# Kernel tuning notes

Hardware: AMD Instinct MI355X
Metric: run time of the kernel (lower is better)

The kernel has to match this reference:

```python
import jax, jax.numpy as jnp
import numpy as np
from jax import lax

B, T, D = 32, 512, 1024
H = 1024
R = 64


def setup_inputs() -> dict:
    key = jax.random.key(0)
    ks = jax.random.split(key, 14)
    s = lambda *sh: 1.0 / np.sqrt(sh[-1])
    inp = {
        "x": jax.random.normal(ks[0], (B, T, D), jnp.float32),
        # sLSTM block params (input_dim=D -> hidden H)
        "Ws": jax.random.normal(ks[1], (4 * H, D), jnp.float32) * s(4 * H, D),
        "bWs": jax.random.normal(ks[2], (4 * H,), jnp.float32) * 0.01,
        "Us": jax.random.normal(ks[3], (4 * H, H), jnp.float32) * s(4 * H, H),
        "bUs": jax.random.normal(ks[4], (4 * H,), jnp.float32) * 0.01,
        "alpha": jnp.ones((H,), jnp.float32),
        # mLSTM block params (input dim = H after first block)
        "Wm": jax.random.normal(ks[5], (4 * H, H), jnp.float32) * s(4 * H, H),
        "bWm": jax.random.normal(ks[6], (4 * H,), jnp.float32) * 0.01,
        "Um": jax.random.normal(ks[7], (4 * H, H), jnp.float32) * s(4 * H, H),
        "bUm": jax.random.normal(ks[8], (4 * H,), jnp.float32) * 0.01,
        "A": jax.random.normal(ks[9], (R, H), jnp.float32) * s(R, H),
        "Bm": jax.random.normal(ks[10], (R, H), jnp.float32) * s(R, H),
        "P": jax.random.normal(ks[11], (H, R), jnp.float32) * s(H, R),
    }
    return inp


def _gates(z):
    i, f, o, g = jnp.split(z, 4, axis=-1)
    return jax.nn.sigmoid(i), jax.nn.sigmoid(f), jax.nn.sigmoid(o), jnp.tanh(g)


def _slstm(x, W, bW, U, bU, alpha):
    b = x.shape[0]
    h0 = jnp.zeros((b, H), x.dtype)
    c0 = jnp.zeros((b, H), x.dtype)
    # precompute the input projection for all timesteps: [T, B, 4H]
    xw = jnp.einsum('btd,kd->tbk', x, W) + bW

    def step(carry, xw_t):
        h, c = carry
        i, f, o, g = _gates(xw_t + h @ U.T + bU)
        c = alpha * (f * c + i * g)
        h = o * jnp.tanh(c)
        return (h, c), h

    _, hs = lax.scan(step, (h0, c0), xw)
    return jnp.swapaxes(hs, 0, 1)  # [B, T, H]


def _mlstm(x, W, bW, U, bU, A, Bm, P):
    b = x.shape[0]
    h0 = jnp.zeros((b, H), x.dtype)
    c0 = jnp.zeros((b, H), x.dtype)
    xw = jnp.einsum('btd,kd->tbk', x, W) + bW     # [T, B, 4H]
    xa = jnp.einsum('btd,rd->tbr', x, A)          # [T, B, R]

    def step(carry, inputs):
        h, c = carry
        xw_t, xa_t = inputs
        i, f, o, g = _gates(xw_t + h @ U.T + bU)
        mix = (xa_t * (h @ Bm.T)) @ P.T           # low-rank mixing -> [B, H]
        c = f * c + i * g + 0.1 * mix
        h = o * jnp.tanh(c)
        return (h, c), h

    _, hs = lax.scan(step, (h0, c0), (xw, xa))
    return jnp.swapaxes(hs, 0, 1)  # [B, T, H]


def reference(x, Ws, bWs, Us, bUs, alpha, Wm, bWm, Um, bUm, A, Bm, P):
    out = _slstm(x, Ws, bWs, Us, bUs, alpha)
    out = _mlstm(out, Wm, bWm, Um, bUm, A, Bm, P)
    return out
```

## Files before the change

### kernel.cpp

```cpp
#include <hip/hip_runtime.h>

#define BB   32
#define TT_  512
#define DD   1024
#define HH   1024
#define RR_  64
#define FH   4096
#define TC   32

typedef __attribute__((ext_vector_type(8))) short          bf16x8;
typedef __attribute__((ext_vector_type(4))) float          f32x4;
typedef __attribute__((ext_vector_type(4))) unsigned short us4;

__device__ __forceinline__ unsigned short f2bf(float x) {
    union { float f; unsigned u; } v; v.f = x;
    return (unsigned short)((v.u + 0x7FFFu + ((v.u >> 16) & 1u)) >> 16);
}

__global__ void init_zero(float4* p, int n4) {
    int i = blockIdx.x * blockDim.x + threadIdx.x;
    if (i < n4) p[i] = make_float4(0.f, 0.f, 0.f, 0.f);
}

__global__ void cvt_bf16(const float* __restrict__ src,
                         unsigned short* __restrict__ dst, int n4) {
    int i = blockIdx.x * blockDim.x + threadIdx.x;
    int stride = gridDim.x * blockDim.x;
    for (; i < n4; i += stride) {
        float4 v = ((const float4*)src)[i];
        us4 t; t.x = f2bf(v.x); t.y = f2bf(v.y); t.z = f2bf(v.z); t.w = f2bf(v.w);
        ((us4*)dst)[i] = t;
    }
}

template<int BM, int BN>
__global__ __launch_bounds__(256) void gemm_mfma(
    const float* __restrict__ Abase, long strideT, long strideB,
    const float* __restrict__ W, const float* __restrict__ bias,
    float* __restrict__ C, int M, int N, int K)
{
    constexpr int BK  = 32;
    constexpr int WTM = BM / 2, WTN = BN / 2;
    constexpr int MI  = WTM / 16, NI = WTN / 16;
    constexpr int AU  = BM * (BK / 4) / 256;
    constexpr int BU  = BN * (BK / 4) / 256;

    __shared__ __align__(16) unsigned short As[BM * BK];
    __shared__ __align__(16) unsigned short Bs[BN * BK];

    const int tid  = threadIdx.x;
    const int lane = tid & 63, wave = tid >> 6;
    const int wm   = wave >> 1, wn = wave & 1;
    const int kg   = lane >> 4;
    const int lr   = lane & 15;
    const long bm  = (long)blockIdx.y * BM;
    const long bn  = (long)blockIdx.x * BN;

    const float* ag[AU]; int alds[AU];
    const float* bg[BU]; int blds[BU];
#pragma unroll
    for (int i = 0; i < AU; ++i) {
        int u = i * 256 + tid, row = u >> 3, uc = u & 7;
        long m = bm + row;
        ag[i]   = Abase + (m >> 5) * strideT + (m & 31) * strideB + uc * 4;
        alds[i] = row * BK + uc * 4;
    }
#pragma unroll
    for (int i = 0; i < BU; ++i) {
        int u = i * 256 + tid, row = u >> 3, uc = u & 7;
        bg[i]   = W + (long)(bn + row) * K + uc * 4;
        blds[i] = row * BK + uc * 4;
    }

    f32x4 acc[MI][NI] = {};

    float4 av[AU], bv[BU];
#pragma unroll
    for (int i = 0; i < AU; ++i) av[i] = *(const float4*)(ag[i]);
#pragma unroll
    for (int i = 0; i < BU; ++i) bv[i] = *(const float4*)(bg[i]);

    for (int k0 = 0; k0 < K; k0 += BK) {
        __syncthreads();
#pragma unroll
        for (int i = 0; i < AU; ++i) {
            us4 t; t.x = f2bf(av[i].x); t.y = f2bf(av[i].y);
                   t.z = f2bf(av[i].z); t.w = f2bf(av[i].w);
            *(us4*)&As[alds[i]] = t;
        }
#pragma unroll
        for (int i = 0; i < BU; ++i) {
            us4 t; t.x = f2bf(bv[i].x); t.y = f2bf(bv[i].y);
                   t.z = f2bf(bv[i].z); t.w = f2bf(bv[i].w);
            *(us4*)&Bs[blds[i]] = t;
        }
        __syncthreads();

        if (k0 + BK < K) {
#pragma unroll
            for (int i = 0; i < AU; ++i) av[i] = *(const float4*)(ag[i] + k0 + BK);
#pragma unroll
            for (int i = 0; i < BU; ++i) bv[i] = *(const float4*)(bg[i] + k0 + BK);
        }

        bf16x8 af[MI], bfr[NI];
#pragma unroll
        for (int mi = 0; mi < MI; ++mi)
            af[mi] = *(const bf16x8*)&As[(wm * WTM + mi * 16 + lr) * BK + kg * 8];
#pragma unroll
        for (int ni = 0; ni < NI; ++ni)
            bfr[ni] = *(const bf16x8*)&Bs[(wn * WTN + ni * 16 + lr) * BK + kg * 8];
#pragma unroll
        for (int mi = 0; mi < MI; ++mi)
#pragma unroll
            for (int ni = 0; ni < NI; ++ni)
                acc[mi][ni] = __builtin_amdgcn_mfma_f32_16x16x32_bf16(
                    af[mi], bfr[ni], acc[mi][ni], 0, 0, 0);
    }

    const int rbase = (lane >> 4) * 4;
#pragma unroll
    for (int mi = 0; mi < MI; ++mi) {
        long m0 = bm + wm * WTM + mi * 16 + rbase;
        long tt = m0 >> 5; int bq = (int)(m0 & 31);
#pragma unroll
        for (int ni = 0; ni < NI; ++ni) {
            long n = bn + wn * WTN + ni * 16 + lr;
            float bia = bias ? bias[n] : 0.f;
            float4 v = make_float4(acc[mi][ni][0] + bia, acc[mi][ni][1] + bia,
                                   acc[mi][ni][2] + bia, acc[mi][ni][3] + bia);
            *(float4*)&C[(tt * N + n) * 32 + bq] = v;
        }
    }
}

__device__ __forceinline__ void slstm_body(
    int bx, const float* __restrict__ xwT,
    const unsigned short* __restrict__ Ubf, const float* __restrict__ bU,
    const float* __restrict__ alpha, const unsigned short* __restrict__ hin,
    unsigned short* __restrict__ hout, float* __restrict__ cst,
    float* __restrict__ out1t, char* smem)
{
    unsigned short* hs = (unsigned short*)smem;
    float* zsl = (float*)(smem + 65536);
    const int tid  = threadIdx.x;
    const int lane = tid & 63, wv = tid >> 6;
    const int j0   = bx * 16;
    const int lr   = lane & 15;
    const int koff = (lane >> 4) << 3;

    const uint4* hg = (const uint4*)hin;
#pragma unroll
    for (int i = 0; i < 16; ++i) {
        int u = tid + (i << 8);
        int o = u << 4;
        int sw = o ^ (((o >> 11) & 7) << 4);
        *(uint4*)(smem + sw) = hg[u];
    }
    __syncthreads();

    const unsigned short* Arow = Ubf + (((long)(wv * HH + j0 + lr)) << 10) + koff;
    const int base0 = lr * 2048 + koff * 2;
    const int base1 = (lr + 16) * 2048 + koff * 2;
    const int swz   = (lr & 7) << 4;

    f32x4 accZ0 = {0.f, 0.f, 0.f, 0.f}, accZ1 = {0.f, 0.f, 0.f, 0.f};
#pragma unroll 4
    for (int k0 = 0; k0 < 1024; k0 += 32) {
        bf16x8 a  = *(const bf16x8*)(Arow + k0);
        bf16x8 b0 = *(const bf16x8*)(smem + ((base0 + k0 * 2) ^ swz));
        bf16x8 b1 = *(const bf16x8*)(smem + ((base1 + k0 * 2) ^ swz));
        accZ0 = __builtin_amdgcn_mfma_f32_16x16x32_bf16(a, b0, accZ0, 0, 0, 0);
        accZ1 = __builtin_amdgcn_mfma_f32_16x16x32_bf16(a, b1, accZ1, 0, 0, 0);
    }
#pragma unroll
    for (int r = 0; r < 4; ++r) {
        int jj = ((lane >> 4) << 2) + r;
        zsl[wv * 512 + jj * 32 + lr]      = accZ0[r];
        zsl[wv * 512 + jj * 32 + lr + 16] = accZ1[r];
    }
    __syncthreads();

#pragma unroll
    for (int rep = 0; rep < 2; ++rep) {
        int p = (rep << 8) + tid;
        int j = p >> 5, b = p & 31;
        int n0 = j0 + j;
        float zi = xwT[(long)n0 * 32 + b]            + zsl[j * 32 + b]        + bU[n0];
        float zf = xwT[(long)(HH + n0) * 32 + b]     + zsl[512 + j * 32 + b]  + bU[HH + n0];
        float zo = xwT[(long)(2 * HH + n0) * 32 + b] + zsl[1024 + j * 32 + b] + bU[2 * HH + n0];
        float zg = xwT[(long)(3 * HH + n0) * 32 + b] + zsl[1536 + j * 32 + b] + bU[3 * HH + n0];
        float ig = 1.f / (1.f + expf(-zi));
        float fg = 1.f / (1.f + expf(-zf));
        float og = 1.f / (1.f + expf(-zo));
        float g  = tanhf(zg);
        float cold = cst[(long)b * HH + n0];
        float cn = alpha[n0] * (fg * cold + ig * g);
        float hn = og * tanhf(cn);
        cst[(long)b * HH + n0]  = cn;
        hout[(long)b * HH + n0] = f2bf(hn);
        out1t[(long)b * HH + n0] = hn;
    }
}

__device__ __forceinline__ void mlstm_body(
    int bx, const float* __restrict__ xwT,
    const unsigned short* __restrict__ Ubf, const float* __restrict__ bU,
    const float* __restrict__ Pmat, const unsigned short* __restrict__ Bmbf,
    const float* __restrict__ xaT, const unsigned short* __restrict__ hin,
    unsigned short* __restrict__ hout, float* __restrict__ cst,
    float* __restrict__ out, int t, char* smem)
{
    unsigned short* hs = (unsigned short*)smem;
    float* zsl = (float*)(smem + 65536);
    float* ssl = (float*)(smem + 65536 + 8192);
    const int tid  = threadIdx.x;
    const int lane = tid & 63, wv = tid >> 6;
    const int j0   = bx * 16;
    const int lr   = lane & 15;
    const int koff = (lane >> 4) << 3;

    const uint4* hg = (const uint4*)hin;
#pragma unroll
    for (int i = 0; i < 16; ++i) {
        int u = tid + (i << 8);
        int o = u << 4;
        int sw = o ^ (((o >> 11) & 7) << 4);
        *(uint4*)(smem + sw) = hg[u];
    }
    __syncthreads();

    const unsigned short* Arow = Ubf + (((long)(wv * HH + j0 + lr)) << 10) + koff;
    const unsigned short* Brow = Bmbf + (((long)(wv * 16 + lr)) << 10) + koff;
    const int base0 = lr * 2048 + koff * 2;
    const int base1 = (lr + 16) * 2048 + koff * 2;
    const int swz   = (lr & 7) << 4;

    f32x4 accZ0 = {0.f, 0.f, 0.f, 0.f}, accZ1 = {0.f, 0.f, 0.f, 0.f};
    f32x4 accS0 = {0.f, 0.f, 0.f, 0.f}, accS1 = {0.f, 0.f, 0.f, 0.f};
#pragma unroll 4
    for (int k0 = 0; k0 < 1024; k0 += 32) {
        bf16x8 a  = *(const bf16x8*)(Arow + k0);
        bf16x8 s  = *(const bf16x8*)(Brow + k0);
        bf16x8 b0 = *(const bf16x8*)(smem + ((base0 + k0 * 2) ^ swz));
        bf16x8 b1 = *(const bf16x8*)(smem + ((base1 + k0 * 2) ^ swz));
        accZ0 = __builtin_amdgcn_mfma_f32_16x16x32_bf16(a, b0, accZ0, 0, 0, 0);
        accZ1 = __builtin_amdgcn_mfma_f32_16x16x32_bf16(a, b1, accZ1, 0, 0, 0);
        accS0 = __builtin_amdgcn_mfma_f32_16x16x32_bf16(s, b0, accS0, 0, 0, 0);
        accS1 = __builtin_amdgcn_mfma_f32_16x16x32_bf16(s, b1, accS1, 0, 0, 0);
    }
#pragma unroll
    for (int r = 0; r < 4; ++r) {
        int jj = ((lane >> 4) << 2) + r;
        zsl[wv * 512 + jj * 32 + lr]      = accZ0[r];
        zsl[wv * 512 + jj * 32 + lr + 16] = accZ1[r];
        ssl[(wv * 16 + jj) * 32 + lr]      = accS0[r];
        ssl[(wv * 16 + jj) * 32 + lr + 16] = accS1[r];
    }
    __syncthreads();

#pragma unroll
    for (int i = 0; i < 8; ++i) {
        int idx = tid + (i << 8);
        ssl[idx] *= xaT[idx];
    }
    __syncthreads();

#pragma unroll
    for (int rep = 0; rep < 2; ++rep) {
        int p = (rep << 8) + tid;
        int j = p >> 5, b = p & 31;
        int n0 = j0 + j;
        float zi = xwT[(long)n0 * 32 + b]            + zsl[j * 32 + b]        + bU[n0];
        float zf = xwT[(long)(HH + n0) * 32 + b]     + zsl[512 + j * 32 + b]  + bU[HH + n0];
        float zo = xwT[(long)(2 * HH + n0) * 32 + b] + zsl[1024 + j * 32 + b] + bU[2 * HH + n0];
        float zg = xwT[(long)(3 * HH + n0) * 32 + b] + zsl[1536 + j * 32 + b] + bU[3 * HH + n0];
        float ig = 1.f / (1.f + expf(-zi));
        float fg = 1.f / (1.f + expf(-zf));
        float og = 1.f / (1.f + expf(-zo));
        float g  = tanhf(zg);
        const float* Pj = Pmat + (long)n0 * 64;
        float mx = 0.f;
#pragma unroll
        for (int r = 0; r < 64; ++r) mx += Pj[r] * ssl[r * 32 + b];
        float cold = cst[(long)b * HH + n0];
        float cn = fg * cold + ig * g + 0.1f * mx;
        float hn = og * tanhf(cn);
        cst[(long)b * HH + n0]  = cn;
        hout[(long)b * HH + n0] = f2bf(hn);
        out[(long)b * (TT_ * HH) + (long)t * HH + n0] = hn;
    }
}

__global__ __launch_bounds__(256) void fused_step(
    const float* __restrict__ xwTs, const unsigned short* __restrict__ UbfS,
    const float* __restrict__ bUs, const float* __restrict__ alpha,
    const unsigned short* __restrict__ hsin, unsigned short* __restrict__ hsout,
    float* __restrict__ cS, float* __restrict__ out1t,
    const float* __restrict__ xwTm, const unsigned short* __restrict__ UbfM,
    const float* __restrict__ bUm, const float* __restrict__ Pmat,
    const unsigned short* __restrict__ Bmbf, const float* __restrict__ xaT,
    const unsigned short* __restrict__ hmin, unsigned short* __restrict__ hmout,
    float* __restrict__ cM, float* __restrict__ out, int t,
    int do_s, int do_m)
{
    __shared__ __align__(16) char smem[81920];
    const int bx = blockIdx.x;
    if (bx < 64) {
        if (do_s)
            slstm_body(bx, xwTs, UbfS, bUs, alpha, hsin, hsout, cS, out1t, smem);
    } else {
        if (do_m)
            mlstm_body(bx - 64, xwTm, UbfM, bUm, Pmat, Bmbf, xaT,
                       hmin, hmout, cM, out, t, smem);
    }
}

extern "C" void kernel_launch(void* const* d_in, const int* in_sizes, int n_in,
                              void* d_out, int out_size, void* d_ws, size_t ws_size,
                              hipStream_t stream) {
    const float* x     = (const float*)d_in[0];
    const float* Ws    = (const float*)d_in[1];
    const float* bWs   = (const float*)d_in[2];
    const float* Us    = (const float*)d_in[3];
    const float* bUs   = (const float*)d_in[4];
    const float* alpha = (const float*)d_in[5];
    const float* Wm    = (const float*)d_in[6];
    const float* bWm   = (const float*)d_in[7];
    const float* Um    = (const float*)d_in[8];
    const float* bUm   = (const float*)d_in[9];
    const float* A     = (const float*)d_in[10];
    const float* Bm    = (const float*)d_in[11];
    const float* P     = (const float*)d_in[12];
    float* out = (float*)d_out;

    float* w      = (float*)d_ws;
    float* xwTs   = w;
    float* xwTm   = xwTs + (long)TC * FH * 32;
    float* out1c  = xwTm + (long)TC * FH * 32;
    float* xaT    = out1c + (long)TC * BB * HH;
    unsigned short* UbfS = (unsigned short*)(xaT + (long)TC * RR_ * 32);
    unsigned short* UbfM = UbfS + (long)FH * HH;
    unsigned short* Bmbf = UbfM + (long)FH * HH;
    unsigned short* hbsA = Bmbf + (long)RR_ * HH;
    unsigned short* hbsB = hbsA + BB * HH;
    unsigned short* hbmA = hbsB + BB * HH;
    unsigned short* hbmB = hbmA + BB * HH;
    float* cS     = (float*)(hbmB + BB * HH);
    float* cM     = cS + BB * HH;

    init_zero<<<128, 256, 0, stream>>>((float4*)hbsA, 32768);

    cvt_bf16<<<2048, 256, 0, stream>>>(Us, UbfS, FH * HH / 4);
    cvt_bf16<<<2048, 256, 0, stream>>>(Um, UbfM, FH * HH / 4);
    cvt_bf16<<<64,   256, 0, stream>>>(Bm, Bmbf, RR_ * HH / 4);

    dim3 gbig(FH / 128, (TC * BB) / 64);
    dim3 gxa(RR_ / 64, (TC * BB) / 64);
    const int NC = TT_ / TC;

    for (int ch = 0; ch <= NC; ++ch) {
        const int do_s = (ch < NC), do_m = (ch > 0);

        if (do_s)
            gemm_mfma<64, 128><<<gbig, 256, 0, stream>>>(
                x + (long)(ch * TC) * DD, (long)DD, (long)TT_ * DD, Ws, bWs,
                xwTs, TC * BB, FH, DD);

        for (int tt = 0; tt < TC; ++tt) {
            const unsigned short* hsin = (tt & 1) ? hbsB : hbsA;
            unsigned short* hsout      = (tt & 1) ? hbsA : hbsB;
            const unsigned short* hmin = (tt & 1) ? hbmB : hbmA;
            unsigned short* hmout      = (tt & 1) ? hbmA : hbmB;
            fused_step<<<128, 256, 0, stream>>>(
                xwTs + (long)tt * FH * 32, UbfS, bUs, alpha,
                hsin, hsout, cS, out1c + (long)tt * BB * HH,
                xwTm + (long)tt * FH * 32, UbfM, bUm, P, Bmbf,
                xaT + (long)tt * RR_ * 32,
                hmin, hmout, cM, out, (ch - 1) * TC + tt,
                do_s, do_m);
        }

        if (do_s) {
            gemm_mfma<64, 128><<<gbig, 256, 0, stream>>>(
                out1c, (long)BB * HH, (long)HH, Wm, bWm,
                xwTm, TC * BB, FH, HH);
            gemm_mfma<64, 64><<<gxa, 256, 0, stream>>>(
                out1c, (long)BB * HH, (long)HH, A, nullptr,
                xaT, TC * BB, RR_, HH);
        }
    }
}
```

Baseline: 8.726 ms.

## Pre-convert GEMM operands to bf16 and fuse Wm and A projections into one GEMM

The input-projection GEMMs now read bf16 operands from pre-converted weights (Ws, Wm, A) and a per-chunk bf16 copy of x. The sLSTM step writes its hidden output directly as bf16. The Wm and A projections are concatenated into one padded weight matrix so a single GEMM produces both xw and xa, with xa read at an offset. The GEMM uses BK=64 with XOR-swizzled shared memory to cut per-iteration fp32-to-bf16 conversion and bank conflicts. This adds extra conversion kernels and workspace but reduces per-chunk launches and memory traffic. The recurrence still dominates runtime.

```diff
diff --git a/kernel.cpp b/kernel.cpp
--- a/kernel.cpp
+++ b/kernel.cpp
@@ -7,6 +7,7 @@
 #define RR_  64
 #define FH   4096
 #define TC   32
+#define NCMB 4224
 
 typedef __attribute__((ext_vector_type(8))) short          bf16x8;
 typedef __attribute__((ext_vector_type(4))) float          f32x4;
@@ -33,17 +34,33 @@
     }
 }
 
+__global__ void fill_bcomb(const float* __restrict__ bWm, float* __restrict__ bcomb) {
+    int i = blockIdx.x * blockDim.x + threadIdx.x;
+    if (i < NCMB) bcomb[i] = (i < FH) ? bWm[i] : 0.f;
+}
+
+__global__ void cvt_x_chunk(const float* __restrict__ x,
+                            unsigned short* __restrict__ xbfc, int t0) {
+    int id = blockIdx.x * blockDim.x + threadIdx.x;
+    for (int u = id; u < 32 * 32 * 256; u += 65536) {
+        int d4 = u & 255, b = (u >> 8) & 31, tt = u >> 13;
+        float4 v = *(const float4*)&x[(((long)b * TT_) + t0 + tt) * DD + (d4 << 2)];
+        us4 o; o.x = f2bf(v.x); o.y = f2bf(v.y); o.z = f2bf(v.z); o.w = f2bf(v.w);
+        *(us4*)&xbfc[(((long)tt * 32 + b) << 10) + (d4 << 2)] = o;
+    }
+}
+
 template<int BM, int BN>
-__global__ __launch_bounds__(256) void gemm_mfma(
-    const float* __restrict__ Abase, long strideT, long strideB,
-    const float* __restrict__ W, const float* __restrict__ bias,
-    float* __restrict__ C, int M, int N, int K)
+__global__ __launch_bounds__(256) void gemm_bf(
+    const unsigned short* __restrict__ Abase, long strideT, long strideB,
+    const unsigned short* __restrict__ W, const float* __restrict__ bias,
+    float* __restrict__ C, int N, int K)
 {
-    constexpr int BK  = 32;
+    constexpr int BK  = 64;
     constexpr int WTM = BM / 2, WTN = BN / 2;
     constexpr int MI  = WTM / 16, NI = WTN / 16;
-    constexpr int AU  = BM * (BK / 4) / 256;
-    constexpr int BU  = BN * (BK / 4) / 256;
+    constexpr int AU  = BM * 8 / 256;
+    constexpr int BU  = BN * 8 / 256;
 
     __shared__ __align__(16) unsigned short As[BM * BK];
     __shared__ __align__(16) unsigned short Bs[BN * BK];
@@ -56,66 +73,72 @@
     const long bm  = (long)blockIdx.y * BM;
     const long bn  = (long)blockIdx.x * BN;
 
-    const float* ag[AU]; int alds[AU];
-    const float* bg[BU]; int blds[BU];
+    const unsigned short* ag[AU]; int ast[AU];
+    const unsigned short* bg[BU]; int bst[BU];
 #pragma unroll
     for (int i = 0; i < AU; ++i) {
         int u = i * 256 + tid, row = u >> 3, uc = u & 7;
         long m = bm + row;
-        ag[i]   = Abase + (m >> 5) * strideT + (m & 31) * strideB + uc * 4;
-        alds[i] = row * BK + uc * 4;
+        ag[i]  = Abase + (m >> 5) * strideT + (m & 31) * strideB + uc * 8;
+        ast[i] = (row * 128 + uc * 16) ^ ((row & 7) << 4);
     }
 #pragma unroll
     for (int i = 0; i < BU; ++i) {
         int u = i * 256 + tid, row = u >> 3, uc = u & 7;
-        bg[i]   = W + (long)(bn + row) * K + uc * 4;
-        blds[i] = row * BK + uc * 4;
+        bg[i]  = W + (long)(bn + row) * K + uc * 8;
+        bst[i] = (row * 128 + uc * 16) ^ ((row & 7) << 4);
     }
 
     f32x4 acc[MI][NI] = {};
 
-    float4 av[AU], bv[BU];
-#pragma unroll
-    for (int i = 0; i < AU; ++i) av[i] = *(const float4*)(ag[i]);
-#pragma unroll
-    for (int i = 0; i < BU; ++i) bv[i] = *(const float4*)(bg[i]);
+    uint4 av[AU], bv[BU];
+#pragma unroll
+    for (int i = 0; i < AU; ++i) av[i] = *(const uint4*)(ag[i]);
+#pragma unroll
+    for (int i = 0; i < BU; ++i) bv[i] = *(const uint4*)(bg[i]);
 
     for (int k0 = 0; k0 < K; k0 += BK) {
         __syncthreads();
 #pragma unroll
-        for (int i = 0; i < AU; ++i) {
-            us4 t; t.x = f2bf(av[i].x); t.y = f2bf(av[i].y);
-                   t.z = f2bf(av[i].z); t.w = f2bf(av[i].w);
-            *(us4*)&As[alds[i]] = t;
-        }
-#pragma unroll
-        for (int i = 0; i < BU; ++i) {
-            us4 t; t.x = f2bf(bv[i].x); t.y = f2bf(bv[i].y);
-                   t.z = f2bf(bv[i].z); t.w = f2bf(bv[i].w);
-            *(us4*)&Bs[blds[i]] = t;
-        }
+        for (int i = 0; i < AU; ++i) *(uint4*)((char*)As + ast[i]) = av[i];
+#pragma unroll
+        for (int i = 0; i < BU; ++i) *(uint4*)((char*)Bs + bst[i]) = bv[i];
         __syncthreads();
 
         if (k0 + BK < K) {
 #pragma unroll
-            for (int i = 0; i < AU; ++i) av[i] = *(const float4*)(ag[i] + k0 + BK);
-#pragma unroll
-            for (int i = 0; i < BU; ++i) bv[i] = *(const float4*)(bg[i] + k0 + BK);
-        }
-
-        bf16x8 af[MI], bfr[NI];
-#pragma unroll
-        for (int mi = 0; mi < MI; ++mi)
-            af[mi] = *(const bf16x8*)&As[(wm * WTM + mi * 16 + lr) * BK + kg * 8];
-#pragma unroll
-        for (int ni = 0; ni < NI; ++ni)
-            bfr[ni] = *(const bf16x8*)&Bs[(wn * WTN + ni * 16 + lr) * BK + kg * 8];
-#pragma unroll
-        for (int mi = 0; mi < MI; ++mi)
-#pragma unroll
-            for (int ni = 0; ni < NI; ++ni)
-                acc[mi][ni] = __builtin_amdgcn_mfma_f32_16x16x32_bf16(
-                    af[mi], bfr[ni], acc[mi][ni], 0, 0, 0);
+            for (int i = 0; i < AU; ++i) av[i] = *(const uint4*)(ag[i] + k0 + BK);
+#pragma unroll
+            for (int i = 0; i < BU; ++i) bv[i] = *(const uint4*)(bg[i] + k0 + BK);
+        }
+
+        bf16x8 af[MI][2], bfr[NI][2];
+#pragma unroll
+        for (int mi = 0; mi < MI; ++mi) {
+            int row = wm * WTM + mi * 16 + lr;
+            int rb = row * 128, sw = (row & 7) << 4;
+#pragma unroll
+            for (int kk = 0; kk < 2; ++kk)
+                af[mi][kk] = *(const bf16x8*)((const char*)As +
+                              (rb + ((kk * 64 + kg * 16) ^ sw)));
+        }
+#pragma unroll
+        for (int ni = 0; ni < NI; ++ni) {
+            int row = wn * WTN + ni * 16 + lr;
+            int rb = row * 128, sw = (row & 7) << 4;
+#pragma unroll
+            for (int kk = 0; kk < 2; ++kk)
+                bfr[ni][kk] = *(const bf16x8*)((const char*)Bs +
+                              (rb + ((kk * 64 + kg * 16) ^ sw)));
+        }
+#pragma unroll
+        for (int kk = 0; kk < 2; ++kk)
+#pragma unroll
+            for (int mi = 0; mi < MI; ++mi)
+#pragma unroll
+                for (int ni = 0; ni < NI; ++ni)
+                    acc[mi][ni] = __builtin_amdgcn_mfma_f32_16x16x32_bf16(
+                        af[mi][kk], bfr[ni][kk], acc[mi][ni], 0, 0, 0);
     }
 
     const int rbase = (lane >> 4) * 4;
@@ -139,9 +162,8 @@
     const unsigned short* __restrict__ Ubf, const float* __restrict__ bU,
     const float* __restrict__ alpha, const unsigned short* __restrict__ hin,
     unsigned short* __restrict__ hout, float* __restrict__ cst,
-    float* __restrict__ out1t, char* smem)
+    unsigned short* __restrict__ out1t, char* smem)
 {
-    unsigned short* hs = (unsigned short*)smem;
     float* zsl = (float*)(smem + 65536);
     const int tid  = threadIdx.x;
     const int lane = tid & 63, wv = tid >> 6;
@@ -197,9 +219,10 @@
         float cold = cst[(long)b * HH + n0];
         float cn = alpha[n0] * (fg * cold + ig * g);
         float hn = og * tanhf(cn);
+        unsigned short hb = f2bf(hn);
         cst[(long)b * HH + n0]  = cn;
-        hout[(long)b * HH + n0] = f2bf(hn);
-        out1t[(long)b * HH + n0] = hn;
+        hout[(long)b * HH + n0] = hb;
+        out1t[(long)b * HH + n0] = hb;
     }
 }
 
@@ -207,13 +230,13 @@
     int bx, const float* __restrict__ xwT,
     const unsigned short* __restrict__ Ubf, const float* __restrict__ bU,
     const float* __restrict__ Pmat, const unsigned short* __restrict__ Bmbf,
-    const float* __restrict__ xaT, const unsigned short* __restrict__ hin,
+    const unsigned short* __restrict__ hin,
     unsigned short* __restrict__ hout, float* __restrict__ cst,
     float* __restrict__ out, int t, char* smem)
 {
-    unsigned short* hs = (unsigned short*)smem;
     float* zsl = (float*)(smem + 65536);
     float* ssl = (float*)(smem + 65536 + 8192);
+    const float* xaT = xwT + (long)FH * 32;
     const int tid  = threadIdx.x;
     const int lane = tid & 63, wv = tid >> 6;
     const int j0   = bx * 16;
@@ -296,10 +319,10 @@
     const float* __restrict__ xwTs, const unsigned short* __restrict__ UbfS,
     const float* __restrict__ bUs, const float* __restrict__ alpha,
     const unsigned short* __restrict__ hsin, unsigned short* __restrict__ hsout,
-    float* __restrict__ cS, float* __restrict__ out1t,
+    float* __restrict__ cS, unsigned short* __restrict__ out1t,
     const float* __restrict__ xwTm, const unsigned short* __restrict__ UbfM,
     const float* __restrict__ bUm, const float* __restrict__ Pmat,
-    const unsigned short* __restrict__ Bmbf, const float* __restrict__ xaT,
+    const unsigned short* __restrict__ Bmbf,
     const unsigned short* __restrict__ hmin, unsigned short* __restrict__ hmout,
     float* __restrict__ cM, float* __restrict__ out, int t,
     int do_s, int do_m)
@@ -311,7 +334,7 @@
             slstm_body(bx, xwTs, UbfS, bUs, alpha, hsin, hsout, cS, out1t, smem);
     } else {
         if (do_m)
-            mlstm_body(bx - 64, xwTm, UbfM, bUm, Pmat, Bmbf, xaT,
+            mlstm_body(bx - 64, xwTm, UbfM, bUm, Pmat, Bmbf,
                        hmin, hmout, cM, out, t, smem);
     }
 }
@@ -334,38 +357,46 @@
     const float* P     = (const float*)d_in[12];
     float* out = (float*)d_out;
 
-    float* w      = (float*)d_ws;
-    float* xwTs   = w;
-    float* xwTm   = xwTs + (long)TC * FH * 32;
-    float* out1c  = xwTm + (long)TC * FH * 32;
-    float* xaT    = out1c + (long)TC * BB * HH;
-    unsigned short* UbfS = (unsigned short*)(xaT + (long)TC * RR_ * 32);
-    unsigned short* UbfM = UbfS + (long)FH * HH;
-    unsigned short* Bmbf = UbfM + (long)FH * HH;
+    float* xwTs  = (float*)d_ws;
+    float* xwTm  = xwTs + (long)TC * FH * 32;
+    float* bcomb = xwTm + (long)TC * NCMB * 32;
+    unsigned short* out1c = (unsigned short*)(bcomb + NCMB);
+    unsigned short* xbfc  = out1c + (long)TC * BB * HH;
+    unsigned short* Wsbf  = xbfc + (long)TC * BB * HH;
+    unsigned short* Wcomb = Wsbf + (long)FH * HH;
+    unsigned short* UbfS  = Wcomb + (long)NCMB * HH;
+    unsigned short* UbfM  = UbfS + (long)FH * HH;
+    unsigned short* Bmbf  = UbfM + (long)FH * HH;
     unsigned short* hbsA = Bmbf + (long)RR_ * HH;
     unsigned short* hbsB = hbsA + BB * HH;
     unsigned short* hbmA = hbsB + BB * HH;
     unsigned short* hbmB = hbmA + BB * HH;
-    float* cS     = (float*)(hbmB + BB * HH);
-    float* cM     = cS + BB * HH;
+    float* cS = (float*)(hbmB + BB * HH);
+    float* cM = cS + BB * HH;
 
     init_zero<<<128, 256, 0, stream>>>((float4*)hbsA, 32768);
 
     cvt_bf16<<<2048, 256, 0, stream>>>(Us, UbfS, FH * HH / 4);
     cvt_bf16<<<2048, 256, 0, stream>>>(Um, UbfM, FH * HH / 4);
     cvt_bf16<<<64,   256, 0, stream>>>(Bm, Bmbf, RR_ * HH / 4);
-
-    dim3 gbig(FH / 128, (TC * BB) / 64);
-    dim3 gxa(RR_ / 64, (TC * BB) / 64);
+    cvt_bf16<<<2048, 256, 0, stream>>>(Ws, Wsbf, FH * HH / 4);
+    cvt_bf16<<<2048, 256, 0, stream>>>(Wm, Wcomb, FH * HH / 4);
+    cvt_bf16<<<64,   256, 0, stream>>>(A, Wcomb + (long)FH * HH, RR_ * HH / 4);
+    init_zero<<<32, 256, 0, stream>>>((float4*)(Wcomb + (long)(FH + RR_) * HH), 8192);
+    fill_bcomb<<<17, 256, 0, stream>>>(bWm, bcomb);
+
+    dim3 gxw(FH / 128, (TC * BB) / 64);
+    dim3 gcm(NCMB / 128, (TC * BB) / 64);
     const int NC = TT_ / TC;
 
     for (int ch = 0; ch <= NC; ++ch) {
         const int do_s = (ch < NC), do_m = (ch > 0);
 
-        if (do_s)
-            gemm_mfma<64, 128><<<gbig, 256, 0, stream>>>(
-                x + (long)(ch * TC) * DD, (long)DD, (long)TT_ * DD, Ws, bWs,
-                xwTs, TC * BB, FH, DD);
+        if (do_s) {
+            cvt_x_chunk<<<256, 256, 0, stream>>>(x, xbfc, ch * TC);
+            gemm_bf<64, 128><<<gxw, 256, 0, stream>>>(
+                xbfc, (long)BB * HH, (long)HH, Wsbf, bWs, xwTs, FH, HH);
+        }
 
         for (int tt = 0; tt < TC; ++tt) {
             const unsigned short* hsin = (tt & 1) ? hbsB : hbsA;
@@ -375,19 +406,14 @@
             fused_step<<<128, 256, 0, stream>>>(
                 xwTs + (long)tt * FH * 32, UbfS, bUs, alpha,
                 hsin, hsout, cS, out1c + (long)tt * BB * HH,
-                xwTm + (long)tt * FH * 32, UbfM, bUm, P, Bmbf,
-                xaT + (long)tt * RR_ * 32,
+                xwTm + (long)tt * NCMB * 32, UbfM, bUm, P, Bmbf,
                 hmin, hmout, cM, out, (ch - 1) * TC + tt,
                 do_s, do_m);
         }
 
         if (do_s) {
-            gemm_mfma<64, 128><<<gbig, 256, 0, stream>>>(
-                out1c, (long)BB * HH, (long)HH, Wm, bWm,
-                xwTm, TC * BB, FH, HH);
-            gemm_mfma<64, 64><<<gxa, 256, 0, stream>>>(
-                out1c, (long)BB * HH, (long)HH, A, nullptr,
-                xaT, TC * BB, RR_, HH);
-        }
-    }
-}
+            gemm_bf<64, 128><<<gcm, 256, 0, stream>>>(
+                out1c, (long)BB * HH, (long)HH, Wcomb, bcomb, xwTm, NCMB, HH);
+        }
+    }
+}
```

After: 10.01 ms. +14.7%, slower.

## Overlap input-projection GEMMs with recurrent steps via extra blocks and bf16 buffers

Applied to the files above, without the earlier changes.

Removes the separate per-chunk Ws/Wm/A GEMM launches. It adds 33 extra blocks to each fused recurrent step, which compute slices of the next chunk's Ws projection and the previous chunk's Wm and A projections, double-buffered so they run alongside the sLSTM and mLSTM recurrences on otherwise idle CUs. The xw projections are also stored in bf16 to cut memory traffic. The risks are slower step kernels, since the extra GEMM blocks add work to the critical serial path, and a loss of precision in the pre-activations.

```diff
diff --git a/kernel.cpp b/kernel.cpp
--- a/kernel.cpp
+++ b/kernel.cpp
@@ -7,6 +7,8 @@
 #define RR_  64
 #define FH   4096
 #define TC   32
+#define NC   16
+#define NW   33
 
 typedef __attribute__((ext_vector_type(8))) short          bf16x8;
 typedef __attribute__((ext_vector_type(4))) float          f32x4;
@@ -15,6 +17,9 @@
 __device__ __forceinline__ unsigned short f2bf(float x) {
     union { float f; unsigned u; } v; v.f = x;
     return (unsigned short)((v.u + 0x7FFFu + ((v.u >> 16) & 1u)) >> 16);
+}
+__device__ __forceinline__ float bf2f(unsigned short u) {
+    union { unsigned u32; float f; } v; v.u32 = ((unsigned)u) << 16; return v.f;
 }
 
 __global__ void init_zero(float4* p, int n4) {
@@ -33,28 +38,29 @@
     }
 }
 
-template<int BM, int BN>
-__global__ __launch_bounds__(256) void gemm_mfma(
+template<int BN, bool OUTBF>
+__device__ __forceinline__ void gemm_body(
+    int bxx, int byy,
     const float* __restrict__ Abase, long strideT, long strideB,
     const float* __restrict__ W, const float* __restrict__ bias,
-    float* __restrict__ C, int M, int N, int K)
+    void* __restrict__ Cout, int N, int K, char* smem)
 {
-    constexpr int BK  = 32;
+    constexpr int BM  = 64, BK = 32;
     constexpr int WTM = BM / 2, WTN = BN / 2;
     constexpr int MI  = WTM / 16, NI = WTN / 16;
     constexpr int AU  = BM * (BK / 4) / 256;
     constexpr int BU  = BN * (BK / 4) / 256;
 
-    __shared__ __align__(16) unsigned short As[BM * BK];
-    __shared__ __align__(16) unsigned short Bs[BN * BK];
+    unsigned short* As = (unsigned short*)smem;
+    unsigned short* Bs = As + BM * BK;
 
     const int tid  = threadIdx.x;
     const int lane = tid & 63, wave = tid >> 6;
     const int wm   = wave >> 1, wn = wave & 1;
     const int kg   = lane >> 4;
     const int lr   = lane & 15;
-    const long bm  = (long)blockIdx.y * BM;
-    const long bn  = (long)blockIdx.x * BN;
+    const long bm  = (long)byy * BM;
+    const long bn  = (long)bxx * BN;
 
     const float* ag[AU]; int alds[AU];
     const float* bg[BU]; int blds[BU];
@@ -122,26 +128,43 @@
 #pragma unroll
     for (int mi = 0; mi < MI; ++mi) {
         long m0 = bm + wm * WTM + mi * 16 + rbase;
-        long tt = m0 >> 5; int bq = (int)(m0 & 31);
+        long trow = m0 >> 5; int bq = (int)(m0 & 31);
 #pragma unroll
         for (int ni = 0; ni < NI; ++ni) {
             long n = bn + wn * WTN + ni * 16 + lr;
             float bia = bias ? bias[n] : 0.f;
-            float4 v = make_float4(acc[mi][ni][0] + bia, acc[mi][ni][1] + bia,
-                                   acc[mi][ni][2] + bia, acc[mi][ni][3] + bia);
-            *(float4*)&C[(tt * N + n) * 32 + bq] = v;
-        }
-    }
+            if (OUTBF) {
+                us4 t; t.x = f2bf(acc[mi][ni][0] + bia);
+                       t.y = f2bf(acc[mi][ni][1] + bia);
+                       t.z = f2bf(acc[mi][ni][2] + bia);
+                       t.w = f2bf(acc[mi][ni][3] + bia);
+                *(us4*)&((unsigned short*)Cout)[(trow * N + n) * 32 + bq] = t;
+            } else {
+                float4 v = make_float4(acc[mi][ni][0] + bia, acc[mi][ni][1] + bia,
+                                       acc[mi][ni][2] + bia, acc[mi][ni][3] + bia);
+                *(float4*)&((float*)Cout)[(trow * N + n) * 32 + bq] = v;
+            }
+        }
+    }
+}
+
+__global__ __launch_bounds__(256) void gemm_pro(
+    const float* __restrict__ Abase, long strideT, long strideB,
+    const float* __restrict__ W, const float* __restrict__ bias,
+    unsigned short* __restrict__ C, int N, int K)
+{
+    __shared__ __align__(16) char smem[12288];
+    gemm_body<128, true>(blockIdx.x, blockIdx.y, Abase, strideT, strideB,
+                         W, bias, C, N, K, smem);
 }
 
 __device__ __forceinline__ void slstm_body(
-    int bx, const float* __restrict__ xwT,
+    int bx, const unsigned short* __restrict__ xwT,
     const unsigned short* __restrict__ Ubf, const float* __restrict__ bU,
     const float* __restrict__ alpha, const unsigned short* __restrict__ hin,
     unsigned short* __restrict__ hout, float* __restrict__ cst,
     float* __restrict__ out1t, char* smem)
 {
-    unsigned short* hs = (unsigned short*)smem;
     float* zsl = (float*)(smem + 65536);
     const int tid  = threadIdx.x;
     const int lane = tid & 63, wv = tid >> 6;
@@ -186,10 +209,10 @@
         int p = (rep << 8) + tid;
         int j = p >> 5, b = p & 31;
         int n0 = j0 + j;
-        float zi = xwT[(long)n0 * 32 + b]            + zsl[j * 32 + b]        + bU[n0];
-        float zf = xwT[(long)(HH + n0) * 32 + b]     + zsl[512 + j * 32 + b]  + bU[HH + n0];
-        float zo = xwT[(long)(2 * HH + n0) * 32 + b] + zsl[1024 + j * 32 + b] + bU[2 * HH + n0];
-        float zg = xwT[(long)(3 * HH + n0) * 32 + b] + zsl[1536 + j * 32 + b] + bU[3 * HH + n0];
+        float zi = bf2f(xwT[(long)n0 * 32 + b])            + zsl[j * 32 + b]        + bU[n0];
+        float zf = bf2f(xwT[(long)(HH + n0) * 32 + b])     + zsl[512 + j * 32 + b]  + bU[HH + n0];
+        float zo = bf2f(xwT[(long)(2 * HH + n0) * 32 + b]) + zsl[1024 + j * 32 + b] + bU[2 * HH + n0];
+        float zg = bf2f(xwT[(long)(3 * HH + n0) * 32 + b]) + zsl[1536 + j * 32 + b] + bU[3 * HH + n0];
         float ig = 1.f / (1.f + expf(-zi));
         float fg = 1.f / (1.f + expf(-zf));
         float og = 1.f / (1.f + expf(-zo));
@@ -204,14 +227,13 @@
 }
 
 __device__ __forceinline__ void mlstm_body(
-    int bx, const float* __restrict__ xwT,
+    int bx, const unsigned short* __restrict__ xwT,
     const unsigned short* __restrict__ Ubf, const float* __restrict__ bU,
     const float* __restrict__ Pmat, const unsigned short* __restrict__ Bmbf,
     const float* __restrict__ xaT, const unsigned short* __restrict__ hin,
     unsigned short* __restrict__ hout, float* __restrict__ cst,
     float* __restrict__ out, int t, char* smem)
 {
-    unsigned short* hs = (unsigned short*)smem;
     float* zsl = (float*)(smem + 65536);
     float* ssl = (float*)(smem + 65536 + 8192);
     const int tid  = threadIdx.x;
@@ -271,10 +293,10 @@
         int p = (rep << 8) + tid;
         int j = p >> 5, b = p & 31;
         int n0 = j0 + j;
-        float zi = xwT[(long)n0 * 32 + b]            + zsl[j * 32 + b]        + bU[n0];
-        float zf = xwT[(long)(HH + n0) * 32 + b]     + zsl[512 + j * 32 + b]  + bU[HH + n0];
-        float zo = xwT[(long)(2 * HH + n0) * 32 + b] + zsl[1024 + j * 32 + b] + bU[2 * HH + n0];
-        float zg = xwT[(long)(3 * HH + n0) * 32 + b] + zsl[1536 + j * 32 + b] + bU[3 * HH + n0];
+        float zi = bf2f(xwT[(long)n0 * 32 + b])            + zsl[j * 32 + b]        + bU[n0];
+        float zf = bf2f(xwT[(long)(HH + n0) * 32 + b])     + zsl[512 + j * 32 + b]  + bU[HH + n0];
+        float zo = bf2f(xwT[(long)(2 * HH + n0) * 32 + b]) + zsl[1024 + j * 32 + b] + bU[2 * HH + n0];
+        float zg = bf2f(xwT[(long)(3 * HH + n0) * 32 + b]) + zsl[1536 + j * 32 + b] + bU[3 * HH + n0];
         float ig = 1.f / (1.f + expf(-zi));
         float fg = 1.f / (1.f + expf(-zf));
         float og = 1.f / (1.f + expf(-zo));
@@ -293,26 +315,55 @@
 }
 
 __global__ __launch_bounds__(256) void fused_step(
-    const float* __restrict__ xwTs, const unsigned short* __restrict__ UbfS,
-    const float* __restrict__ bUs, const float* __restrict__ alpha,
-    const unsigned short* __restrict__ hsin, unsigned short* __restrict__ hsout,
-    float* __restrict__ cS, float* __restrict__ out1t,
-    const float* __restrict__ xwTm, const unsigned short* __restrict__ UbfM,
-    const float* __restrict__ bUm, const float* __restrict__ Pmat,
-    const unsigned short* __restrict__ Bmbf, const float* __restrict__ xaT,
-    const unsigned short* __restrict__ hmin, unsigned short* __restrict__ hmout,
-    float* __restrict__ cM, float* __restrict__ out, int t,
-    int do_s, int do_m)
+    const unsigned short* xwTs_r, const unsigned short* UbfS,
+    const float* bUs, const float* alpha,
+    const unsigned short* hsin, unsigned short* hsout, float* cS, float* out1t,
+    const unsigned short* xwTm_r, const unsigned short* UbfM, const float* bUm,
+    const float* Pmat, const unsigned short* Bmbf, const float* xaT_r,
+    const unsigned short* hmin, unsigned short* hmout, float* cM,
+    float* out, int t,
+    const float* xnext, const float* Ws, const float* bWs,
+    const float* Wm, const float* bWm, const float* Amat,
+    const float* out1c,
+    unsigned short* xwTs_w, unsigned short* xwTm_wc, unsigned short* xwTm_wp,
+    float* xaT_wc, float* xaT_wp,
+    int tt, int do_s, int do_m, int wm_cur_ok, int wm_prev_ok, int xw_ok)
 {
     __shared__ __align__(16) char smem[81920];
     const int bx = blockIdx.x;
     if (bx < 64) {
         if (do_s)
-            slstm_body(bx, xwTs, UbfS, bUs, alpha, hsin, hsout, cS, out1t, smem);
+            slstm_body(bx, xwTs_r, UbfS, bUs, alpha, hsin, hsout, cS, out1t, smem);
+    } else if (bx < 128) {
+        if (do_m)
+            mlstm_body(bx - 64, xwTm_r, UbfM, bUm, Pmat, Bmbf, xaT_r,
+                       hmin, hmout, cM, out, t, smem);
     } else {
-        if (do_m)
-            mlstm_body(bx - 64, xwTm, UbfM, bUm, Pmat, Bmbf, xaT,
-                       hmin, hmout, cM, out, t, smem);
+        const int w = bx - 128;
+        const int even = !(tt & 1);
+        const int nWm = even ? 17 : 16;
+        if (w < nWm) {
+            const int q = even ? w : 17 + w;
+            const int prevband = (tt < 2);
+            const int pair = prevband ? 15 : ((tt >> 1) - 1);
+            const int ok = prevband ? wm_prev_ok : wm_cur_ok;
+            if (ok) {
+                unsigned short* xwTm_t = prevband ? xwTm_wp : xwTm_wc;
+                float* xaT_t           = prevband ? xaT_wp : xaT_wc;
+                if (q < 32)
+                    gemm_body<128, true>(q, pair, out1c, (long)BB * HH, (long)HH,
+                                         Wm, bWm, xwTm_t, FH, HH, smem);
+                else
+                    gemm_body<64, false>(0, pair, out1c, (long)BB * HH, (long)HH,
+                                         Amat, nullptr, xaT_t, RR_, HH, smem);
+            }
+        } else {
+            const int done = 33 * (tt >> 1) + ((tt & 1) ? 16 : 0);
+            const int k = done + (w - nWm);
+            if (k < 512 && xw_ok)
+                gemm_body<128, true>(k & 31, k >> 5, xnext, (long)DD,
+                                     (long)TT_ * DD, Ws, bWs, xwTs_w, FH, DD, smem);
+        }
     }
 }
 
@@ -334,20 +385,22 @@
     const float* P     = (const float*)d_in[12];
     float* out = (float*)d_out;
 
-    float* w      = (float*)d_ws;
-    float* xwTs   = w;
-    float* xwTm   = xwTs + (long)TC * FH * 32;
-    float* out1c  = xwTm + (long)TC * FH * 32;
-    float* xaT    = out1c + (long)TC * BB * HH;
-    unsigned short* UbfS = (unsigned short*)(xaT + (long)TC * RR_ * 32);
-    unsigned short* UbfM = UbfS + (long)FH * HH;
-    unsigned short* Bmbf = UbfM + (long)FH * HH;
-    unsigned short* hbsA = Bmbf + (long)RR_ * HH;
+    unsigned short* xwTs0 = (unsigned short*)d_ws;
+    unsigned short* xwTs1 = xwTs0 + (long)TC * FH * 32;
+    unsigned short* xwTm0 = xwTs1 + (long)TC * FH * 32;
+    unsigned short* xwTm1 = xwTm0 + (long)TC * FH * 32;
+    unsigned short* UbfS  = xwTm1 + (long)TC * FH * 32;
+    unsigned short* UbfM  = UbfS + (long)FH * HH;
+    unsigned short* Bmbf  = UbfM + (long)FH * HH;
+    float* out1c = (float*)(Bmbf + (long)RR_ * HH);
+    float* xaT0  = out1c + (long)TC * BB * HH;
+    float* xaT1  = xaT0 + (long)TC * RR_ * 32;
+    unsigned short* hbsA = (unsigned short*)(xaT1 + (long)TC * RR_ * 32);
     unsigned short* hbsB = hbsA + BB * HH;
     unsigned short* hbmA = hbsB + BB * HH;
     unsigned short* hbmB = hbmA + BB * HH;
-    float* cS     = (float*)(hbmB + BB * HH);
-    float* cM     = cS + BB * HH;
+    float* cS = (float*)(hbmB + BB * HH);
+    float* cM = cS + BB * HH;
 
     init_zero<<<128, 256, 0, stream>>>((float4*)hbsA, 32768);
 
@@ -355,39 +408,40 @@
     cvt_bf16<<<2048, 256, 0, stream>>>(Um, UbfM, FH * HH / 4);
     cvt_bf16<<<64,   256, 0, stream>>>(Bm, Bmbf, RR_ * HH / 4);
 
-    dim3 gbig(FH / 128, (TC * BB) / 64);
-    dim3 gxa(RR_ / 64, (TC * BB) / 64);
-    const int NC = TT_ / TC;
-
-    for (int ch = 0; ch <= NC; ++ch) {
-        const int do_s = (ch < NC), do_m = (ch > 0);
-
-        if (do_s)
-            gemm_mfma<64, 128><<<gbig, 256, 0, stream>>>(
-                x + (long)(ch * TC) * DD, (long)DD, (long)TT_ * DD, Ws, bWs,
-                xwTs, TC * BB, FH, DD);
+    gemm_pro<<<dim3(32, 16), 256, 0, stream>>>(
+        x, (long)DD, (long)TT_ * DD, Ws, bWs, xwTs0, FH, DD);
+
+    unsigned short* xwTsBuf[2] = {xwTs0, xwTs1};
+    unsigned short* xwTmBuf[2] = {xwTm0, xwTm1};
+    float* xaTBuf[2] = {xaT0, xaT1};
+
+    for (int p = 0; p <= NC; ++p) {
+        const int do_s = (p < NC), do_m = (p > 0);
+        const int wm_cur_ok  = (p < NC);
+        const int wm_prev_ok = (p > 0);
+        const int xw_ok      = (p + 1 < NC);
+        const float* xnext = x + (long)(p + 1) * TC * DD;
+        unsigned short* xwTs_r = xwTsBuf[p & 1];
+        unsigned short* xwTs_w = xwTsBuf[(p + 1) & 1];
+        unsigned short* xwTm_r = xwTmBuf[(p + 1) & 1];
+        unsigned short* xwTm_wc = xwTmBuf[p & 1];
+        float* xaT_r  = xaTBuf[(p + 1) & 1];
+        float* xaT_wc = xaTBuf[p & 1];
 
         for (int tt = 0; tt < TC; ++tt) {
             const unsigned short* hsin = (tt & 1) ? hbsB : hbsA;
             unsigned short* hsout      = (tt & 1) ? hbsA : hbsB;
             const unsigned short* hmin = (tt & 1) ? hbmB : hbmA;
             unsigned short* hmout      = (tt & 1) ? hbmA : hbmB;
-            fused_step<<<128, 256, 0, stream>>>(
-                xwTs + (long)tt * FH * 32, UbfS, bUs, alpha,
+            fused_step<<<128 + NW, 256, 0, stream>>>(
+                xwTs_r + (long)tt * FH * 32, UbfS, bUs, alpha,
                 hsin, hsout, cS, out1c + (long)tt * BB * HH,
-                xwTm + (long)tt * FH * 32, UbfM, bUm, P, Bmbf,
-                xaT + (long)tt * RR_ * 32,
-                hmin, hmout, cM, out, (ch - 1) * TC + tt,
-                do_s, do_m);
-        }
-
-        if (do_s) {
-            gemm_mfma<64, 128><<<gbig, 256, 0, stream>>>(
-                out1c, (long)BB * HH, (long)HH, Wm, bWm,
-                xwTm, TC * BB, FH, HH);
-            gemm_mfma<64, 64><<<gxa, 256, 0, stream>>>(
-                out1c, (long)BB * HH, (long)HH, A, nullptr,
-                xaT, TC * BB, RR_, HH);
-        }
-    }
-}
+                xwTm_r + (long)tt * FH * 32, UbfM, bUm, P, Bmbf,
+                xaT_r + (long)tt * RR_ * 32,
+                hmin, hmout, cM, out, (p - 1) * TC + tt,
+                xnext, Ws, bWs, Wm, bWm, A, out1c,
+                xwTs_w, xwTm_wc, xwTm_r, xaT_wc, xaT_r,
+                tt, do_s, do_m, wm_cur_ok, wm_prev_ok, xw_ok);
+        }
+    }
+}
```

Result: slower. 16.27 ms (+86.5%).
